# Optimization experiments

Measured on AMD Instinct MI355X. Metric: run time of the kernel, lower is better.

The kernel has to match this reference:

```python
import jax, jax.numpy as jnp
import numpy as np

N, E, D, G, FP = 20000, 320000, 1280, 64, 65


def _glorot(k, shape):
    s = jnp.sqrt(6.0 / (shape[0] + shape[1])).astype(jnp.float32)
    return jax.random.uniform(k, shape, jnp.float32, -s, s)


def setup_inputs() -> dict:
    key = jax.random.key(0)
    ks = jax.random.split(key, 16)
    return {
        'x': jax.random.normal(ks[0], (N, D), jnp.float32),
        'edge_index': jax.random.randint(ks[1], (2, E), 0, N),
        'batch': jnp.sort(jax.random.randint(ks[2], (N,), 0, G)),
        'fp_x': jax.random.normal(ks[3], (G, FP), jnp.float32),
        'W1': _glorot(ks[4], (D, D)), 'b1': jnp.zeros((D,), jnp.float32),
        'W2': _glorot(ks[5], (D, 640)), 'b2': jnp.zeros((640,), jnp.float32),
        'W3': _glorot(ks[6], (640, 320)), 'b3': jnp.zeros((320,), jnp.float32),
        'Wg1': _glorot(ks[7], (320, 1024)), 'bg1': jnp.zeros((1024,), jnp.float32),
        'Wg2': _glorot(ks[8], (1024, 128)), 'bg2': jnp.zeros((128,), jnp.float32),
        'Wf1': _glorot(ks[9], (193, 1024)), 'bf1': jnp.zeros((1024,), jnp.float32),
        'Wf2': _glorot(ks[10], (1024, 512)), 'bf2': jnp.zeros((512,), jnp.float32),
        'Wo': _glorot(ks[11], (512, 1)), 'bo': jnp.zeros((1,), jnp.float32),
    }


def reference(x, edge_index, batch, fp_x, W1, b1, W2, b2, W3, b3,
              Wg1, bg1, Wg2, bg2, Wf1, bf1, Wf2, bf2, Wo, bo):
    n = x.shape[0]
    g = fp_x.shape[0]
    loop = jnp.arange(n)
    src = jnp.concatenate([edge_index[0], loop])  # self-loops added (GCNConv default)
    dst = jnp.concatenate([edge_index[1], loop])
    deg = jax.ops.segment_sum(jnp.ones_like(dst, x.dtype), dst, num_segments=n)
    dis = jnp.where(deg > 0, jax.lax.rsqrt(deg), 0.0)
    norm = dis[src] * dis[dst]  # D^-1/2 (A+I) D^-1/2 edge weights

    def gcn(h, W, b):
        h = h @ W                                  # transform first (PyG GCNConv)
        agg = jax.ops.segment_sum(h[src] * norm[:, None], dst, num_segments=n)
        return agg + b

    xt = jax.nn.relu(gcn(x, W1, b1))
    xt = jax.nn.relu(gcn(xt, W2, b2))
    xt = jax.nn.relu(gcn(xt, W3, b3))
    # global mean pool over graphs
    s = jax.ops.segment_sum(xt, batch, num_segments=g)
    cnt = jax.ops.segment_sum(jnp.ones((n,), xt.dtype), batch, num_segments=g)
    xt = s / jnp.maximum(cnt, 1.0)[:, None]
    # MLP head (dropout in eval mode -> identity)
    xt = jax.nn.relu(xt @ Wg1 + bg1)
    xt = xt @ Wg2 + bg2
    xc = jnp.concatenate([fp_x, xt], axis=1)       # [G, 65+128=193]
    xc = jax.nn.relu(xc @ Wf1 + bf1)
    xc = jax.nn.relu(xc @ Wf2 + bf2)
    return xc @ Wo + bo
```

## Files before the change

### kernel.cpp

```cpp
#include <hip/hip_runtime.h>
#include <hip/hip_bf16.h>

#define N_NODES 20000
#define NPAD    20224
#define N_EDGES 320000
#define NGRAPH  64
#define FPD     65

typedef __attribute__((ext_vector_type(8))) __bf16 bf16x8;
typedef __attribute__((ext_vector_type(4))) float floatx4;
typedef __attribute__((ext_vector_type(8))) ushort ushort8v;

__device__ inline float bf2f(ushort u) {
    union { unsigned int i; float f; } c; c.i = ((unsigned int)u) << 16; return c.f;
}
__device__ inline ushort f2bf(float v) {
    __hip_bfloat16 h = __float2bfloat16(v);
    return *(ushort*)&h;
}
__device__ __forceinline__ void gld_lds16(const ushort* g, ushort* l) {
    __builtin_amdgcn_global_load_lds(
        (const __attribute__((address_space(1))) unsigned int*)g,
        (__attribute__((address_space(3))) unsigned int*)l,
        16, 0, 0);
}

__global__ void init_cnt(int* cnt) {
    int i = blockIdx.x * blockDim.x + threadIdx.x;
    if (i < N_NODES) cnt[i] = 1;
}
__global__ void count_in(const int* __restrict__ dst, int* cnt) {
    int e = blockIdx.x * blockDim.x + threadIdx.x;
    if (e < N_EDGES) atomicAdd(&cnt[dst[e]], 1);
}
__global__ __launch_bounds__(1024) void scan_offsets(const int* __restrict__ cnt,
                                                     int* __restrict__ off, int* __restrict__ cursor,
                                                     float* __restrict__ dis) {
    __shared__ int part[1024];
    int t = threadIdx.x;
    const int chunk = (N_NODES + 1023) / 1024;
    int lo = t * chunk, hi = min(lo + chunk, N_NODES);
    int s = 0;
    for (int i = lo; i < hi; ++i) s += (cnt[i] + 3) & ~3;
    part[t] = s;
    __syncthreads();
    for (int d = 1; d < 1024; d <<= 1) {
        int v = (t >= d) ? part[t - d] : 0;
        __syncthreads();
        part[t] += v;
        __syncthreads();
    }
    int base = part[t] - s;
    for (int i = lo; i < hi; ++i) {
        int c = cnt[i];
        off[i] = base; cursor[i] = base;
        dis[i] = rsqrtf((float)c);
        base += (c + 3) & ~3;
    }
    if (t == 1023) off[N_NODES] = part[1023];
}
__global__ void fill_csr(const int* __restrict__ src, const int* __restrict__ dst,
                         const float* __restrict__ dis, int* cursor,
                         int* __restrict__ esrc, float* __restrict__ ew) {
    int e = blockIdx.x * blockDim.x + threadIdx.x;
    if (e >= N_EDGES + N_NODES) return;
    int s, d; float w;
    if (e < N_EDGES) { s = src[e]; d = dst[e]; w = dis[s] * dis[d]; }
    else { s = d = e - N_EDGES; w = dis[s] * dis[s]; }
    int pos = atomicAdd(&cursor[d], 1);
    esrc[pos] = s; ew[pos] = w;
}
__global__ void fill_pad(const int* __restrict__ off, const int* __restrict__ cursor,
                         int* __restrict__ esrc, float* __restrict__ ew) {
    int i = blockIdx.x * blockDim.x + threadIdx.x;
    if (i >= N_NODES) return;
    int e1 = off[i + 1];
    for (int e = cursor[i]; e < e1; ++e) { esrc[e] = i; ew[e] = 0.f; }
}

__global__ void conv_f32_bf16_tiled(const float* __restrict__ in, ushort* __restrict__ out) {
    int idx = blockIdx.x * blockDim.x + threadIdx.x;
    if (idx >= N_NODES * 320) return;
    int n = idx / 320, f4 = idx % 320;
    float4 v = *(const float4*)(in + (size_t)n * 1280 + f4 * 4);
    ushort4 o;
    o.x = f2bf(v.x); o.y = f2bf(v.y); o.z = f2bf(v.z); o.w = f2bf(v.w);
    *(ushort4*)(out + (size_t)(f4 >> 4) * (NPAD * 64) + (size_t)n * 64 + (f4 & 15) * 4) = o;
}
__global__ void transpose_conv(const float* __restrict__ W, ushort* __restrict__ Wt,
                               int K, int Nc, int KP) {
    __shared__ float t[32][33];
    int k0 = blockIdx.x * 32, n0 = blockIdx.y * 32;
    int tx = threadIdx.x, ty = threadIdx.y;
    #pragma unroll
    for (int i = 0; i < 4; ++i)
        t[ty + i * 8][tx] = W[(size_t)(k0 + ty + i * 8) * Nc + n0 + tx];
    __syncthreads();
    #pragma unroll
    for (int i = 0; i < 4; ++i)
        Wt[(size_t)(n0 + ty + i * 8) * KP + k0 + tx] = f2bf(t[tx][ty + i * 8]);
}


#define STAGE128(AsB, BsB, kt) do {                                                   \
    const ushort* Ak_ = A + (size_t)(kt) * (NPAD * 64);                               \
    const ushort* Bk_ = Bt + (size_t)(kt) * 64;                                       \
    _Pragma("unroll")                                                                 \
    for (int i_ = 0; i_ < 4; ++i_) {                                                  \
        int c_ = tid + i_ * 256;                                                      \
        int row_ = c_ >> 3, g_ = c_ & 7;                                              \
        gld_lds16(Ak_ + (size_t)(bm + row_) * 64 + (g_ ^ (row_ & 7)) * 8, &AsB[c_ * 8]); \
    }                                                                                 \
    _Pragma("unroll")                                                                 \
    for (int i_ = 0; i_ < 4; ++i_) {                                                  \
        int c_ = tid + i_ * 256;                                                      \
        int row_ = c_ >> 3, g_ = c_ & 7;                                              \
        gld_lds16(Bk_ + (size_t)(bn + row_) * KP + (g_ ^ (row_ & 7)) * 8, &BsB[c_ * 8]); \
    }                                                                                 \
} while (0)

#define COMPUTE128(AsB, BsB) do {                                                     \
    _Pragma("unroll")                                                                 \
    for (int ks = 0; ks < 2; ++ks) {                                                  \
        bf16x8 af[4], bfv[4];                                                         \
        _Pragma("unroll")                                                             \
        for (int t = 0; t < 4; ++t) {                                                 \
            int ra = wr * 64 + t * 16 + mr;                                           \
            af[t] = *(const bf16x8*)&AsB[ra * 64 + ((ks * 4 + quad) ^ (ra & 7)) * 8]; \
            int rb = wc * 64 + t * 16 + mr;                                           \
            bfv[t] = *(const bf16x8*)&BsB[rb * 64 + ((ks * 4 + quad) ^ (rb & 7)) * 8];\
        }                                                                             \
        _Pragma("unroll")                                                             \
        for (int tm = 0; tm < 4; ++tm)                                                \
            _Pragma("unroll")                                                         \
            for (int tn = 0; tn < 4; ++tn)                                            \
                acc[tm][tn] = __builtin_amdgcn_mfma_f32_16x16x32_bf16(af[tm], bfv[tn], acc[tm][tn], 0, 0, 0); \
    }                                                                                 \
} while (0)

__global__ __launch_bounds__(256) void gemm_bf16_128(
    const ushort* __restrict__ A, const ushort* __restrict__ Bt,
    ushort* __restrict__ C, int M, int K, int KP, int Nc, int nt, int total, int chunk)
{
    __shared__ ushort As0[128 * 64], As1[128 * 64];
    __shared__ ushort Bs0[128 * 64], Bs1[128 * 64];
    const int bi = blockIdx.x;
    const int tile = (bi & 7) * chunk + (bi >> 3);
    if (tile >= total) return;
    const int bm = (tile / nt) * 128, bn = (tile % nt) * 128;

    const int tid = threadIdx.x;
    const int wid = tid >> 6, lane = tid & 63;
    const int wr = wid >> 1, wc = wid & 1;
    const int quad = lane >> 4, mr = lane & 15;

    floatx4 acc[4][4];
    #pragma unroll
    for (int i = 0; i < 4; ++i)
        #pragma unroll
        for (int j = 0; j < 4; ++j)
            acc[i][j] = (floatx4){0.f, 0.f, 0.f, 0.f};

    const int NT = K >> 6;
    STAGE128(As0, Bs0, 0);
    __syncthreads();
    for (int kt = 0; kt < NT; kt += 2) {
        if (kt + 1 < NT) STAGE128(As1, Bs1, kt + 1);
        COMPUTE128(As0, Bs0);
        __syncthreads();
        if (kt + 1 < NT) {
            if (kt + 2 < NT) STAGE128(As0, Bs0, kt + 2);
            COMPUTE128(As1, Bs1);
            __syncthreads();
        }
    }

    ushort* Cc = C + (size_t)((bn >> 6) + wc) * (NPAD * 64);
    #pragma unroll
    for (int tm = 0; tm < 4; ++tm) {
        int rowb = bm + wr * 64 + tm * 16 + quad * 4;
        #pragma unroll
        for (int r = 0; r < 4; ++r) {
            int row = rowb + r;
            if (row < M) {
                #pragma unroll
                for (int tn = 0; tn < 4; ++tn)
                    Cc[(size_t)row * 64 + tn * 16 + mr] = f2bf(acc[tm][tn][r]);
            }
        }
    }
}

#define STAGE64(AsB, BsB, kt) do {                                                    \
    const ushort* Ak_ = A + (size_t)(kt) * (NPAD * 64);                               \
    const ushort* Bk_ = Bt + (size_t)(kt) * 64;                                       \
    _Pragma("unroll")                                                                 \
    for (int i_ = 0; i_ < 8; ++i_) {                                                  \
        int c_ = tid + i_ * 256;                                                      \
        int row_ = c_ >> 3, g_ = c_ & 7;                                              \
        gld_lds16(Ak_ + (size_t)(bm + row_) * 64 + (g_ ^ (row_ & 7)) * 8, &AsB[c_ * 8]); \
    }                                                                                 \
    _Pragma("unroll")                                                                 \
    for (int i_ = 0; i_ < 2; ++i_) {                                                  \
        int c_ = tid + i_ * 256;                                                      \
        int row_ = c_ >> 3, g_ = c_ & 7;                                              \
        gld_lds16(Bk_ + (size_t)(bn + row_) * KP + (g_ ^ (row_ & 7)) * 8, &BsB[c_ * 8]); \
    }                                                                                 \
} while (0)

#define COMPUTE64(AsB, BsB) do {                                                      \
    _Pragma("unroll")                                                                 \
    for (int ks = 0; ks < 2; ++ks) {                                                  \
        bf16x8 af[4], bfv[4];                                                         \
        _Pragma("unroll")                                                             \
        for (int t = 0; t < 4; ++t) {                                                 \
            int ra = wid * 64 + t * 16 + mr;                                          \
            af[t] = *(const bf16x8*)&AsB[ra * 64 + ((ks * 4 + quad) ^ (ra & 7)) * 8]; \
            int rb = t * 16 + mr;                                                     \
            bfv[t] = *(const bf16x8*)&BsB[rb * 64 + ((ks * 4 + quad) ^ (rb & 7)) * 8];\
        }                                                                             \
        _Pragma("unroll")                                                             \
        for (int tm = 0; tm < 4; ++tm)                                                \
            _Pragma("unroll")                                                         \
            for (int tn = 0; tn < 4; ++tn)                                            \
                acc[tm][tn] = __builtin_amdgcn_mfma_f32_16x16x32_bf16(af[tm], bfv[tn], acc[tm][tn], 0, 0, 0); \
    }                                                                                 \
} while (0)

__global__ __launch_bounds__(256) void gemm_bf16(
    const ushort* __restrict__ A, const ushort* __restrict__ Bt,
    ushort* __restrict__ C, int M, int K, int KP, int Nc, int nt, int total, int chunk)
{
    __shared__ ushort As0[256 * 64], As1[256 * 64];
    __shared__ ushort Bs0[64 * 64], Bs1[64 * 64];
    const int bi = blockIdx.x;
    const int tile = (bi & 7) * chunk + (bi >> 3);
    if (tile >= total) return;
    const int bm = (tile / nt) * 256, bn = (tile % nt) * 64;

    const int tid = threadIdx.x;
    const int wid = tid >> 6, lane = tid & 63;
    const int quad = lane >> 4, mr = lane & 15;

    floatx4 acc[4][4];
    #pragma unroll
    for (int i = 0; i < 4; ++i)
        #pragma unroll
        for (int j = 0; j < 4; ++j)
            acc[i][j] = (floatx4){0.f, 0.f, 0.f, 0.f};

    const int NT = K >> 6;
    STAGE64(As0, Bs0, 0);
    __syncthreads();
    for (int kt = 0; kt < NT; kt += 2) {
        if (kt + 1 < NT) STAGE64(As1, Bs1, kt + 1);
        COMPUTE64(As0, Bs0);
        __syncthreads();
        if (kt + 1 < NT) {
            if (kt + 2 < NT) STAGE64(As0, Bs0, kt + 2);
            COMPUTE64(As1, Bs1);
            __syncthreads();
        }
    }

    ushort* Cc = C + (size_t)(bn >> 6) * (NPAD * 64);
    #pragma unroll
    for (int tm = 0; tm < 4; ++tm) {
        int rowb = bm + wid * 64 + tm * 16 + quad * 4;
        #pragma unroll
        for (int r = 0; r < 4; ++r) {
            int row = rowb + r;
            if (row < M) {
                #pragma unroll
                for (int tn = 0; tn < 4; ++tn)
                    Cc[(size_t)row * 64 + tn * 16 + mr] = f2bf(acc[tm][tn][r]);
            }
        }
    }
}

static inline void launch_gemm(const ushort* A, const ushort* Bt, ushort* C,
                               int M, int K, int KP, int Nc, hipStream_t stream) {
    if (Nc % 128 == 0) {
        int mt = (M + 127) / 128, nt = Nc / 128;
        int total = mt * nt;
        int chunk = (total + 7) / 8;
        gemm_bf16_128<<<8 * chunk, 256, 0, stream>>>(A, Bt, C, M, K, KP, Nc, nt, total, chunk);
    } else {
        int mt = (M + 255) / 256, nt = Nc / 64;
        int total = mt * nt;
        int chunk = (total + 7) / 8;
        gemm_bf16<<<8 * chunk, 256, 0, stream>>>(A, Bt, C, M, K, KP, Nc, nt, total, chunk);
    }
}

template<int TPN>
__global__ __launch_bounds__(256) void gather_tiled(
    const ushort* __restrict__ h, const int* __restrict__ off,
    const int* __restrict__ esrc, const float* __restrict__ ew,
    const float* __restrict__ bias, ushort* __restrict__ out_bf,
    float* __restrict__ out_f32, int wbf, int wf32, int nchunks, int nbpc)
{
    constexpr int NPB = 256 / TPN;
    const int bi = blockIdx.x;
    const int xcd = bi & 7;
    const int t2 = bi >> 3;
    const int s = t2 / nbpc, nb = t2 - s * nbpc;
    const int c = s * 8 + xcd;
    if (c >= nchunks) return;
    const int tid = threadIdx.x;
    const int g = tid / TPN, t = tid % TPN;
    const int n = nb * NPB + g;
    if (n >= N_NODES) return;

    const ushort* hc = h + (size_t)c * (NPAD * 64) + t * 8;
    float acc[8];
    #pragma unroll
    for (int j = 0; j < 8; ++j) acc[j] = 0.f;

    const int e0 = off[n], e1 = off[n + 1];
    for (int e = e0; e < e1; e += 4) {
        int4   s4 = *(const int4*)(esrc + e);
        float4 w4 = *(const float4*)(ew + e);
        ushort8v v0 = *(const ushort8v*)(hc + (size_t)s4.x * 64);
        ushort8v v1 = *(const ushort8v*)(hc + (size_t)s4.y * 64);
        ushort8v v2 = *(const ushort8v*)(hc + (size_t)s4.z * 64);
        ushort8v v3 = *(const ushort8v*)(hc + (size_t)s4.w * 64);
        #pragma unroll
        for (int j = 0; j < 8; ++j)
            acc[j] += w4.x * bf2f(v0[j]) + w4.y * bf2f(v1[j])
                    + w4.z * bf2f(v2[j]) + w4.w * bf2f(v3[j]);
    }

    const int fb = c * 64 + t * 8;
    float4 b0 = *(const float4*)(bias + fb);
    float4 b1 = *(const float4*)(bias + fb + 4);
    float r[8];
    r[0] = fmaxf(acc[0] + b0.x, 0.f); r[1] = fmaxf(acc[1] + b0.y, 0.f);
    r[2] = fmaxf(acc[2] + b0.z, 0.f); r[3] = fmaxf(acc[3] + b0.w, 0.f);
    r[4] = fmaxf(acc[4] + b1.x, 0.f); r[5] = fmaxf(acc[5] + b1.y, 0.f);
    r[6] = fmaxf(acc[6] + b1.z, 0.f); r[7] = fmaxf(acc[7] + b1.w, 0.f);
    if (wbf) {
        ushort8v o;
        #pragma unroll
        for (int j = 0; j < 8; ++j) o[j] = f2bf(r[j]);
        *(ushort8v*)(out_bf + (size_t)c * (NPAD * 64) + (size_t)n * 64 + t * 8) = o;
    }
    if (wf32) {
        *(float4*)(out_f32 + (size_t)n * (nchunks * 64) + fb)     = make_float4(r[0], r[1], r[2], r[3]);
        *(float4*)(out_f32 + (size_t)n * (nchunks * 64) + fb + 4) = make_float4(r[4], r[5], r[6], r[7]);
    }
}

static inline void launch_gather(const ushort* h, const int* off, const int* esrc,
                                 const float* ew, const float* bias, ushort* out_bf,
                                 float* out_f32, int wbf, int wf32, int nchunks,
                                 hipStream_t stream) {
    constexpr int TPN = 8;
    constexpr int NPB = 256 / TPN;
    const int nbpc = (N_NODES + NPB - 1) / NPB;
    const int sblocks = (nchunks + 7) / 8;
    gather_tiled<TPN><<<8 * sblocks * nbpc, 256, 0, stream>>>(
        h, off, esrc, ew, bias, out_bf, out_f32, wbf, wf32, nchunks, nbpc);
}

__global__ void graph_bounds(const int* __restrict__ batch, int* __restrict__ gstart) {
    int n = blockIdx.x * blockDim.x + threadIdx.x;
    if (n >= N_NODES) return;
    int b = batch[n];
    int bp = (n == 0) ? -1 : batch[n - 1];
    for (int g = bp + 1; g <= b; ++g) gstart[g] = n;
    if (n == N_NODES - 1)
        for (int g = b + 1; g <= NGRAPH; ++g) gstart[g] = N_NODES;
}
__global__ __launch_bounds__(320) void pool_graph(
    const float* __restrict__ x, const int* __restrict__ gstart, float* __restrict__ pool)
{
    int g = blockIdx.x;
    int t = threadIdx.x;
    int s = gstart[g], e = gstart[g + 1];
    float a0 = 0.f, a1 = 0.f, a2 = 0.f, a3 = 0.f;
    int n = s;
    for (; n + 3 < e; n += 4) {
        a0 += x[(size_t)(n + 0) * 320 + t];
        a1 += x[(size_t)(n + 1) * 320 + t];
        a2 += x[(size_t)(n + 2) * 320 + t];
        a3 += x[(size_t)(n + 3) * 320 + t];
    }
    for (; n < e; ++n) a0 += x[(size_t)n * 320 + t];
    float acc = (a0 + a1) + (a2 + a3);
    pool[g * 320 + t] = acc / fmaxf((float)(e - s), 1.0f);
}

template<int K, int SPLIT, int RELU>
__global__ __launch_bounds__(256) void head_gemm_sk(
    const float* __restrict__ in, int istride,
    const float* __restrict__ W, const float* __restrict__ b,
    float* __restrict__ out, int M, int Nc)
{
    constexpr int KQ = K / SPLIT;
    int idx = blockIdx.x * blockDim.x + threadIdx.x;
    int oi = idx / SPLIT, r = idx % SPLIT;
    if (oi >= M * Nc) return;
    int m = oi / Nc, c = oi % Nc;
    const float* ip = in + (size_t)m * istride + r * KQ;
    const float* wp = W + (size_t)r * KQ * Nc + c;
    float a0 = 0.f, a1 = 0.f, a2 = 0.f, a3 = 0.f;
    #pragma unroll
    for (int k = 0; k < KQ; k += 4) {
        float4 v = *(const float4*)(ip + k);
        a0 += v.x * wp[(size_t)(k + 0) * Nc];
        a1 += v.y * wp[(size_t)(k + 1) * Nc];
        a2 += v.z * wp[(size_t)(k + 2) * Nc];
        a3 += v.w * wp[(size_t)(k + 3) * Nc];
    }
    float s = (a0 + a1) + (a2 + a3);
    #pragma unroll
    for (int o = 1; o < SPLIT; o <<= 1) s += __shfl_xor(s, o, 64);
    if (r == 0) {
        s += b[c];
        out[oi] = RELU ? fmaxf(s, 0.f) : s;
    }
}

__global__ void head_prep(const float* __restrict__ fp, const float* __restrict__ xt,
                          float* __restrict__ xc, const float* __restrict__ Wf1,
                          float* __restrict__ Wp) {
    int idx = blockIdx.x * blockDim.x + threadIdx.x;
    if (idx < 208 * 1024) {
        int k = idx / 1024;
        Wp[idx] = (k < 193) ? Wf1[idx] : 0.f;
    }
    if (idx < NGRAPH * 208) {
        int g = idx / 208, j = idx % 208;
        float v = 0.f;
        if (j < FPD) v = fp[g * FPD + j];
        else if (j < 193) v = xt[g * 128 + (j - FPD)];
        xc[idx] = v;
    }
}

__global__ __launch_bounds__(256) void head_out(
    const float* __restrict__ f2, const float* __restrict__ Wo,
    const float* __restrict__ bo, float* __restrict__ out)
{
    int m = blockIdx.x;
    int t = threadIdx.x;
    float2 v = *(const float2*)(f2 + (size_t)m * 512 + t * 2);
    float2 w = *(const float2*)(Wo + t * 2);
    float s = v.x * w.x + v.y * w.y;
    #pragma unroll
    for (int o = 32; o > 0; o >>= 1) s += __shfl_down(s, o, 64);
    __shared__ float ps[4];
    if ((t & 63) == 0) ps[t >> 6] = s;
    __syncthreads();
    if (t == 0) out[m] = ps[0] + ps[1] + ps[2] + ps[3] + bo[0];
}

extern "C" void kernel_launch(void* const* d_in, const int* in_sizes, int n_in,
                              void* d_out, int out_size, void* d_ws, size_t ws_size,
                              hipStream_t stream) {
    const float* x    = (const float*)d_in[0];
    const int*   eidx = (const int*)d_in[1];
    const int*   batch= (const int*)d_in[2];
    const float* fp_x = (const float*)d_in[3];
    const float* W1 = (const float*)d_in[4];  const float* b1 = (const float*)d_in[5];
    const float* W2 = (const float*)d_in[6];  const float* b2 = (const float*)d_in[7];
    const float* W3 = (const float*)d_in[8];  const float* b3 = (const float*)d_in[9];
    const float* Wg1= (const float*)d_in[10]; const float* bg1= (const float*)d_in[11];
    const float* Wg2= (const float*)d_in[12]; const float* bg2= (const float*)d_in[13];
    const float* Wf1= (const float*)d_in[14]; const float* bf1= (const float*)d_in[15];
    const float* Wf2= (const float*)d_in[16]; const float* bf2= (const float*)d_in[17];
    const float* Wo = (const float*)d_in[18]; const float* bo = (const float*)d_in[19];
    float* out = (float*)d_out;

    const int* src = eidx;
    const int* dst = eidx + N_EDGES;

    char* p = (char*)d_ws;
    float* dis   = (float*)p;  p += 20480 * 4;
    int*   cntI  = (int*)p;    p += 20480 * 4;
    int*   off   = (int*)p;    p += 20480 * 4;
    int*   cursor= (int*)p;    p += 20480 * 4;
    int*   gstart= (int*)p;    p += 128 * 4;
    int*   esrc  = (int*)p;    p += 402432 * 4;
    float* ew    = (float*)p;  p += 402432 * 4;
    ushort* xbf  = (ushort*)p; p += (size_t)NPAD * 1280 * 2;
    ushort* hbf  = (ushort*)p; p += (size_t)NPAD * 1280 * 2;
    ushort* abf  = (ushort*)p; p += (size_t)NPAD * 1280 * 2;
    float* a3f   = (float*)p;  p += (size_t)N_NODES * 320 * 4;
    ushort* Wt   = (ushort*)p; p += (size_t)1280 * 1344 * 2;
    float* pool  = (float*)p;  p += NGRAPH * 320 * 4;
    float* m1    = (float*)p;  p += NGRAPH * 1024 * 4;
    float* m2    = (float*)p;  p += NGRAPH * 128 * 4;
    float* xc    = (float*)p;  p += NGRAPH * 208 * 4;
    float* f1    = (float*)p;  p += NGRAPH * 1024 * 4;
    float* f2    = (float*)p;  p += NGRAPH * 512 * 4;
    float* Wf1p  = (float*)p;  p += 208 * 1024 * 4;

    init_cnt<<<(N_NODES + 255) / 256, 256, 0, stream>>>(cntI);
    count_in<<<(N_EDGES + 255) / 256, 256, 0, stream>>>(dst, cntI);
    scan_offsets<<<1, 1024, 0, stream>>>(cntI, off, cursor, dis);
    fill_csr<<<(N_EDGES + N_NODES + 255) / 256, 256, 0, stream>>>(src, dst, dis, cursor, esrc, ew);
    fill_pad<<<(N_NODES + 255) / 256, 256, 0, stream>>>(off, cursor, esrc, ew);
    graph_bounds<<<(N_NODES + 255) / 256, 256, 0, stream>>>(batch, gstart);

    {
        conv_f32_bf16_tiled<<<(N_NODES * 320 + 255) / 256, 256, 0, stream>>>(x, xbf);
        transpose_conv<<<dim3(1280 / 32, 1280 / 32), dim3(32, 8), 0, stream>>>(W1, Wt, 1280, 1280, 1344);
        launch_gemm(xbf, Wt, hbf, N_NODES, 1280, 1344, 1280, stream);
        launch_gather(hbf, off, esrc, ew, b1, abf, (float*)nullptr, 1, 0, 20, stream);
    }
    {
        transpose_conv<<<dim3(1280 / 32, 640 / 32), dim3(32, 8), 0, stream>>>(W2, Wt, 1280, 640, 1344);
        launch_gemm(abf, Wt, hbf, N_NODES, 1280, 1344, 640, stream);
        launch_gather(hbf, off, esrc, ew, b2, abf, (float*)nullptr, 1, 0, 10, stream);
    }
    {
        transpose_conv<<<dim3(640 / 32, 320 / 32), dim3(32, 8), 0, stream>>>(W3, Wt, 640, 320, 704);
        launch_gemm(abf, Wt, hbf, N_NODES, 640, 704, 320, stream);
        launch_gather(hbf, off, esrc, ew, b3, (ushort*)nullptr, a3f, 0, 1, 5, stream);
    }

    pool_graph<<<NGRAPH, 320, 0, stream>>>(a3f, gstart, pool);

    head_gemm_sk<320, 4, 1><<<(NGRAPH * 1024 * 4 + 255) / 256, 256, 0, stream>>>(pool, 320, Wg1, bg1, m1, NGRAPH, 1024);
    head_gemm_sk<1024, 8, 0><<<(NGRAPH * 128 * 8 + 255) / 256, 256, 0, stream>>>(m1, 1024, Wg2, bg2, m2, NGRAPH, 128);
    head_prep<<<(208 * 1024 + 255) / 256, 256, 0, stream>>>(fp_x, m2, xc, Wf1, Wf1p);
    head_gemm_sk<208, 4, 1><<<(NGRAPH * 1024 * 4 + 255) / 256, 256, 0, stream>>>(xc, 208, Wf1p, bf1, f1, NGRAPH, 1024);
    head_gemm_sk<1024, 8, 1><<<(NGRAPH * 512 * 8 + 255) / 256, 256, 0, stream>>>(f1, 1024, Wf2, bf2, f2, NGRAPH, 512);
    head_out<<<NGRAPH, 256, 0, stream>>>(f2, Wo, bo, out);
}
```

Before: 700.4 us.

## Merge prep kernels into one launch, split pooling, fuse head concat and mean scaling

Folds the x conversion, all three weight transposes, Wf1 padding, fp_x copy and graph-bounds computation into a single multi-role prep kernel, and gives each layer its own transposed-weight buffer. The separate count-init kernel becomes a memset, with the self-loop +1 moved into the scan. Pooling is split four ways per graph with atomic accumulation, and the mean division moves into the first head GEMM. The second head GEMM now writes directly into the concat buffer, which removes head_prep. The aim is fewer launches and more parallel pooling, at the cost of a larger workspace and nondeterministic float atomic sums.

```diff
diff --git a/kernel.cpp b/kernel.cpp
--- a/kernel.cpp
+++ b/kernel.cpp
@@ -25,10 +25,6 @@
         16, 0, 0);
 }
 
-__global__ void init_cnt(int* cnt) {
-    int i = blockIdx.x * blockDim.x + threadIdx.x;
-    if (i < N_NODES) cnt[i] = 1;
-}
 __global__ void count_in(const int* __restrict__ dst, int* cnt) {
     int e = blockIdx.x * blockDim.x + threadIdx.x;
     if (e < N_EDGES) atomicAdd(&cnt[dst[e]], 1);
@@ -41,7 +37,7 @@
     const int chunk = (N_NODES + 1023) / 1024;
     int lo = t * chunk, hi = min(lo + chunk, N_NODES);
     int s = 0;
-    for (int i = lo; i < hi; ++i) s += (cnt[i] + 3) & ~3;
+    for (int i = lo; i < hi; ++i) s += (cnt[i] + 4) & ~3;
     part[t] = s;
     __syncthreads();
     for (int d = 1; d < 1024; d <<= 1) {
@@ -52,7 +48,7 @@
     }
     int base = part[t] - s;
     for (int i = lo; i < hi; ++i) {
-        int c = cnt[i];
+        int c = cnt[i] + 1;
         off[i] = base; cursor[i] = base;
         dis[i] = rsqrtf((float)c);
         base += (c + 3) & ~3;
@@ -78,27 +74,69 @@
     for (int e = cursor[i]; e < e1; ++e) { esrc[e] = i; ew[e] = 0.f; }
 }
 
-__global__ void conv_f32_bf16_tiled(const float* __restrict__ in, ushort* __restrict__ out) {
-    int idx = blockIdx.x * blockDim.x + threadIdx.x;
-    if (idx >= N_NODES * 320) return;
-    int n = idx / 320, f4 = idx % 320;
-    float4 v = *(const float4*)(in + (size_t)n * 1280 + f4 * 4);
-    ushort4 o;
-    o.x = f2bf(v.x); o.y = f2bf(v.y); o.z = f2bf(v.z); o.w = f2bf(v.w);
-    *(ushort4*)(out + (size_t)(f4 >> 4) * (NPAD * 64) + (size_t)n * 64 + (f4 & 15) * 4) = o;
-}
-__global__ void transpose_conv(const float* __restrict__ W, ushort* __restrict__ Wt,
-                               int K, int Nc, int KP) {
-    __shared__ float t[32][33];
-    int k0 = blockIdx.x * 32, n0 = blockIdx.y * 32;
-    int tx = threadIdx.x, ty = threadIdx.y;
-    #pragma unroll
-    for (int i = 0; i < 4; ++i)
-        t[ty + i * 8][tx] = W[(size_t)(k0 + ty + i * 8) * Nc + n0 + tx];
-    __syncthreads();
-    #pragma unroll
-    for (int i = 0; i < 4; ++i)
-        Wt[(size_t)(n0 + ty + i * 8) * KP + k0 + tx] = f2bf(t[tx][ty + i * 8]);
+__global__ __launch_bounds__(256) void prep_mega(
+    const float* __restrict__ x, ushort* __restrict__ xbf,
+    const float* __restrict__ W1, ushort* __restrict__ Wt1,
+    const float* __restrict__ W2, ushort* __restrict__ Wt2,
+    const float* __restrict__ W3, ushort* __restrict__ Wt3,
+    const float* __restrict__ Wf1, float* __restrict__ Wf1p,
+    const float* __restrict__ fp, float* __restrict__ xc,
+    const int* __restrict__ batch, int* __restrict__ gstart)
+{
+    __shared__ float tsh[32][33];
+    int b = blockIdx.x;
+    if (b < 25000) {
+        int idx = b * 256 + threadIdx.x;
+        int n = idx / 320, f4 = idx % 320;
+        float4 v = *(const float4*)(x + (size_t)n * 1280 + f4 * 4);
+        ushort4 o;
+        o.x = f2bf(v.x); o.y = f2bf(v.y); o.z = f2bf(v.z); o.w = f2bf(v.w);
+        *(ushort4*)(xbf + (size_t)(f4 >> 4) * (NPAD * 64) + (size_t)n * 64 + (f4 & 15) * 4) = o;
+        return;
+    }
+    b -= 25000;
+    if (b < 2600) {
+        const float* W; ushort* Wt; int Nc, KP, kt, nt;
+        if (b < 1600)      { W = W1; Wt = Wt1; Nc = 1280; KP = 1344; kt = b % 40; nt = b / 40; }
+        else if (b < 2400) { int b2 = b - 1600; W = W2; Wt = Wt2; Nc = 640; KP = 1344; kt = b2 % 40; nt = b2 / 40; }
+        else               { int b2 = b - 2400; W = W3; Wt = Wt3; Nc = 320; KP = 704;  kt = b2 % 20; nt = b2 / 20; }
+        int k0 = kt * 32, n0 = nt * 32;
+        int tx = threadIdx.x & 31, ty = threadIdx.x >> 5;
+        #pragma unroll
+        for (int i = 0; i < 4; ++i)
+            tsh[ty + i * 8][tx] = W[(size_t)(k0 + ty + i * 8) * Nc + n0 + tx];
+        __syncthreads();
+        #pragma unroll
+        for (int i = 0; i < 4; ++i)
+            Wt[(size_t)(n0 + ty + i * 8) * KP + k0 + tx] = f2bf(tsh[tx][ty + i * 8]);
+        return;
+    }
+    b -= 2600;
+    if (b < 832) {
+        int idx = b * 256 + threadIdx.x;
+        int k = idx / 1024;
+        Wf1p[idx] = (k < 193) ? Wf1[idx] : 0.f;
+        return;
+    }
+    b -= 832;
+    if (b < 52) {
+        int idx = b * 256 + threadIdx.x;
+        if (idx < NGRAPH * 208) {
+            int g = idx / 208, j = idx % 208;
+            xc[idx] = (j < FPD) ? fp[g * FPD + j] : 0.f;
+        }
+        return;
+    }
+    b -= 52;
+    {
+        int n = b * 256 + threadIdx.x;
+        if (n >= N_NODES) return;
+        int bb = batch[n];
+        int bp = (n == 0) ? -1 : batch[n - 1];
+        for (int g = bp + 1; g <= bb; ++g) gstart[g] = n;
+        if (n == N_NODES - 1)
+            for (int g = bb + 1; g <= NGRAPH; ++g) gstart[g] = N_NODES;
+    }
 }
 
 
@@ -364,39 +402,32 @@
         h, off, esrc, ew, bias, out_bf, out_f32, wbf, wf32, nchunks, nbpc);
 }
 
-__global__ void graph_bounds(const int* __restrict__ batch, int* __restrict__ gstart) {
-    int n = blockIdx.x * blockDim.x + threadIdx.x;
-    if (n >= N_NODES) return;
-    int b = batch[n];
-    int bp = (n == 0) ? -1 : batch[n - 1];
-    for (int g = bp + 1; g <= b; ++g) gstart[g] = n;
-    if (n == N_NODES - 1)
-        for (int g = b + 1; g <= NGRAPH; ++g) gstart[g] = N_NODES;
-}
-__global__ __launch_bounds__(320) void pool_graph(
+__global__ __launch_bounds__(320) void pool_partial(
     const float* __restrict__ x, const int* __restrict__ gstart, float* __restrict__ pool)
 {
-    int g = blockIdx.x;
+    int g = blockIdx.x, q = blockIdx.y;
     int t = threadIdx.x;
-    int s = gstart[g], e = gstart[g + 1];
+    int s = gstart[g], e = gstart[g + 1], len = e - s;
+    int lo = s + (len * q) / 4, hi = s + (len * (q + 1)) / 4;
     float a0 = 0.f, a1 = 0.f, a2 = 0.f, a3 = 0.f;
-    int n = s;
-    for (; n + 3 < e; n += 4) {
+    int n = lo;
+    for (; n + 3 < hi; n += 4) {
         a0 += x[(size_t)(n + 0) * 320 + t];
         a1 += x[(size_t)(n + 1) * 320 + t];
         a2 += x[(size_t)(n + 2) * 320 + t];
         a3 += x[(size_t)(n + 3) * 320 + t];
     }
-    for (; n < e; ++n) a0 += x[(size_t)n * 320 + t];
+    for (; n < hi; ++n) a0 += x[(size_t)n * 320 + t];
     float acc = (a0 + a1) + (a2 + a3);
-    pool[g * 320 + t] = acc / fmaxf((float)(e - s), 1.0f);
-}
-
-template<int K, int SPLIT, int RELU>
+    if (hi > lo) atomicAdd(&pool[g * 320 + t], acc);
+}
+
+template<int K, int SPLIT, int RELU, int SCALE>
 __global__ __launch_bounds__(256) void head_gemm_sk(
     const float* __restrict__ in, int istride,
     const float* __restrict__ W, const float* __restrict__ b,
-    float* __restrict__ out, int M, int Nc)
+    float* __restrict__ out, int M, int Nc, int ostride, int ooff,
+    const int* __restrict__ gs)
 {
     constexpr int KQ = K / SPLIT;
     int idx = blockIdx.x * blockDim.x + threadIdx.x;
@@ -418,25 +449,12 @@
     #pragma unroll
     for (int o = 1; o < SPLIT; o <<= 1) s += __shfl_xor(s, o, 64);
     if (r == 0) {
+        if (SCALE) {
+            float len = (float)(gs[m + 1] - gs[m]);
+            s *= 1.f / fmaxf(len, 1.f);
+        }
         s += b[c];
-        out[oi] = RELU ? fmaxf(s, 0.f) : s;
-    }
-}
-
-__global__ void head_prep(const float* __restrict__ fp, const float* __restrict__ xt,
-                          float* __restrict__ xc, const float* __restrict__ Wf1,
-                          float* __restrict__ Wp) {
-    int idx = blockIdx.x * blockDim.x + threadIdx.x;
-    if (idx < 208 * 1024) {
-        int k = idx / 1024;
-        Wp[idx] = (k < 193) ? Wf1[idx] : 0.f;
-    }
-    if (idx < NGRAPH * 208) {
-        int g = idx / 208, j = idx % 208;
-        float v = 0.f;
-        if (j < FPD) v = fp[g * FPD + j];
-        else if (j < 193) v = xt[g * 128 + (j - FPD)];
-        xc[idx] = v;
+        out[(size_t)m * ostride + ooff + c] = RELU ? fmaxf(s, 0.f) : s;
     }
 }
 
@@ -489,45 +507,43 @@
     ushort* hbf  = (ushort*)p; p += (size_t)NPAD * 1280 * 2;
     ushort* abf  = (ushort*)p; p += (size_t)NPAD * 1280 * 2;
     float* a3f   = (float*)p;  p += (size_t)N_NODES * 320 * 4;
-    ushort* Wt   = (ushort*)p; p += (size_t)1280 * 1344 * 2;
+    ushort* Wt1  = (ushort*)p; p += (size_t)1280 * 1344 * 2;
+    ushort* Wt2  = (ushort*)p; p += (size_t)640 * 1344 * 2;
+    ushort* Wt3  = (ushort*)p; p += (size_t)320 * 704 * 2;
     float* pool  = (float*)p;  p += NGRAPH * 320 * 4;
     float* m1    = (float*)p;  p += NGRAPH * 1024 * 4;
-    float* m2    = (float*)p;  p += NGRAPH * 128 * 4;
     float* xc    = (float*)p;  p += NGRAPH * 208 * 4;
     float* f1    = (float*)p;  p += NGRAPH * 1024 * 4;
     float* f2    = (float*)p;  p += NGRAPH * 512 * 4;
     float* Wf1p  = (float*)p;  p += 208 * 1024 * 4;
 
-    init_cnt<<<(N_NODES + 255) / 256, 256, 0, stream>>>(cntI);
+    hipMemsetAsync(cntI, 0, N_NODES * 4, stream);
+    hipMemsetAsync(pool, 0, NGRAPH * 320 * 4, stream);
+
+    prep_mega<<<25000 + 2600 + 832 + 52 + 79, 256, 0, stream>>>(
+        x, xbf, W1, Wt1, W2, Wt2, W3, Wt3, Wf1, Wf1p, fp_x, xc, batch, gstart);
+
     count_in<<<(N_EDGES + 255) / 256, 256, 0, stream>>>(dst, cntI);
     scan_offsets<<<1, 1024, 0, stream>>>(cntI, off, cursor, dis);
     fill_csr<<<(N_EDGES + N_NODES + 255) / 256, 256, 0, stream>>>(src, dst, dis, cursor, esrc, ew);
     fill_pad<<<(N_NODES + 255) / 256, 256, 0, stream>>>(off, cursor, esrc, ew);
-    graph_bounds<<<(N_NODES + 255) / 256, 256, 0, stream>>>(batch, gstart);
-
-    {
-        conv_f32_bf16_tiled<<<(N_NODES * 320 + 255) / 256, 256, 0, stream>>>(x, xbf);
-        transpose_conv<<<dim3(1280 / 32, 1280 / 32), dim3(32, 8), 0, stream>>>(W1, Wt, 1280, 1280, 1344);
-        launch_gemm(xbf, Wt, hbf, N_NODES, 1280, 1344, 1280, stream);
-        launch_gather(hbf, off, esrc, ew, b1, abf, (float*)nullptr, 1, 0, 20, stream);
-    }
-    {
-        transpose_conv<<<dim3(1280 / 32, 640 / 32), dim3(32, 8), 0, stream>>>(W2, Wt, 1280, 640, 1344);
-        launch_gemm(abf, Wt, hbf, N_NODES, 1280, 1344, 640, stream);
-        launch_gather(hbf, off, esrc, ew, b2, abf, (float*)nullptr, 1, 0, 10, stream);
-    }
-    {
-        transpose_conv<<<dim3(640 / 32, 320 / 32), dim3(32, 8), 0, stream>>>(W3, Wt, 640, 320, 704);
-        launch_gemm(abf, Wt, hbf, N_NODES, 640, 704, 320, stream);
-        launch_gather(hbf, off, esrc, ew, b3, (ushort*)nullptr, a3f, 0, 1, 5, stream);
-    }
-
-    pool_graph<<<NGRAPH, 320, 0, stream>>>(a3f, gstart, pool);
-
-    head_gemm_sk<320, 4, 1><<<(NGRAPH * 1024 * 4 + 255) / 256, 256, 0, stream>>>(pool, 320, Wg1, bg1, m1, NGRAPH, 1024);
-    head_gemm_sk<1024, 8, 0><<<(NGRAPH * 128 * 8 + 255) / 256, 256, 0, stream>>>(m1, 1024, Wg2, bg2, m2, NGRAPH, 128);
-    head_prep<<<(208 * 1024 + 255) / 256, 256, 0, stream>>>(fp_x, m2, xc, Wf1, Wf1p);
-    head_gemm_sk<208, 4, 1><<<(NGRAPH * 1024 * 4 + 255) / 256, 256, 0, stream>>>(xc, 208, Wf1p, bf1, f1, NGRAPH, 1024);
-    head_gemm_sk<1024, 8, 1><<<(NGRAPH * 512 * 8 + 255) / 256, 256, 0, stream>>>(f1, 1024, Wf2, bf2, f2, NGRAPH, 512);
+
+    launch_gemm(xbf, Wt1, hbf, N_NODES, 1280, 1344, 1280, stream);
+    launch_gather(hbf, off, esrc, ew, b1, abf, (float*)nullptr, 1, 0, 20, stream);
+    launch_gemm(abf, Wt2, hbf, N_NODES, 1280, 1344, 640, stream);
+    launch_gather(hbf, off, esrc, ew, b2, abf, (float*)nullptr, 1, 0, 10, stream);
+    launch_gemm(abf, Wt3, hbf, N_NODES, 640, 704, 320, stream);
+    launch_gather(hbf, off, esrc, ew, b3, (ushort*)nullptr, a3f, 0, 1, 5, stream);
+
+    pool_partial<<<dim3(NGRAPH, 4), 320, 0, stream>>>(a3f, gstart, pool);
+
+    head_gemm_sk<320, 4, 1, 1><<<(NGRAPH * 1024 * 4 + 255) / 256, 256, 0, stream>>>(
+        pool, 320, Wg1, bg1, m1, NGRAPH, 1024, 1024, 0, gstart);
+    head_gemm_sk<1024, 8, 0, 0><<<(NGRAPH * 128 * 8 + 255) / 256, 256, 0, stream>>>(
+        m1, 1024, Wg2, bg2, xc, NGRAPH, 128, 208, FPD, (const int*)nullptr);
+    head_gemm_sk<208, 4, 1, 0><<<(NGRAPH * 1024 * 4 + 255) / 256, 256, 0, stream>>>(
+        xc, 208, Wf1p, bf1, f1, NGRAPH, 1024, 1024, 0, (const int*)nullptr);
+    head_gemm_sk<1024, 8, 1, 0><<<(NGRAPH * 512 * 8 + 255) / 256, 256, 0, stream>>>(
+        f1, 1024, Wf2, bf2, f2, NGRAPH, 512, 512, 0, (const int*)nullptr);
     head_out<<<NGRAPH, 256, 0, stream>>>(f2, Wo, bo, out);
 }
```

Result: no change. 698.7 us (-0.2%).
